# Kernel tuning notes

Measured on AMD Instinct MI355X. Metric: run time of the kernel, lower is better.

## Reference

```python
import jax, jax.numpy as jnp
import numpy as np

N, F, H, D = 50000, 128, 8, 16   # nodes, node features, heads, per-head dim (F == H*D -> Identity residual)
E, G = 800000, 512               # edges, graphs
HD = H * D


def _xavier(key, shape):
    fan = sum(shape[-2:]) if len(shape) >= 2 else shape[0] + 1
    lim = (6.0 / (shape[-2] + shape[-1])) ** 0.5 if len(shape) >= 2 else (6.0 / fan) ** 0.5
    return jax.random.uniform(key, shape, jnp.float32, -lim, lim)


def setup_inputs() -> dict:
    key = jax.random.key(0)
    ks = jax.random.split(key, 10)
    x = jax.random.normal(ks[0], (N, F), jnp.float32)
    edge_index = jax.random.randint(ks[1], (2, E), 0, N, dtype=jnp.int64)
    batch = jnp.sort(jax.random.randint(ks[2], (N,), 0, G, dtype=jnp.int64))
    W_src = _xavier(ks[3], (HD, F))
    W_dst = _xavier(ks[4], (HD, F))
    double_attn = _xavier(ks[5], (1, H, D))  # xavier over last two dims
    bias = jnp.zeros((HD,), jnp.float32)
    prelu_alpha = jnp.float32(0.25)          # nn.PReLU() default single weight
    w_weighting = _xavier(ks[6], (1, HD))
    b_weighting = jnp.zeros((1,), jnp.float32)
    w_score = _xavier(ks[7], (HD, HD))
    b_score = jnp.zeros((HD,), jnp.float32)
    return {
        "x": x, "edge_index": edge_index, "batch": batch,
        "W_src": W_src, "W_dst": W_dst, "double_attn": double_attn,
        "bias": bias, "prelu_alpha": prelu_alpha,
        "w_weighting": w_weighting, "b_weighting": b_weighting,
        "w_score": w_score, "b_score": b_score,
    }


def reference(x, edge_index, batch, W_src, W_dst, double_attn, bias, prelu_alpha,
              w_weighting, b_weighting, w_score, b_score):
    src, dst = edge_index[0], edge_index[1]
    # dropout is identity in eval mode
    src_p = (x @ W_src.T).reshape(N, H, D)    # [N,H,D]
    dst_p = (x @ W_dst.T).reshape(N, H, D)
    # edge-wise attention logits: gather + LeakyReLU(0.2) + dot with attention vector
    e = src_p[src] + dst_p[dst]               # [E,H,D]
    e = jnp.where(e > 0, e, 0.2 * e)
    logits = jnp.einsum('ehd,ohd->eh', e, double_attn)  # [E,H] (double_attn has leading 1)
    # segment softmax over destination nodes (global max shift, as in original)
    exp = jnp.exp(logits - logits.max())
    denom = jax.ops.segment_sum(exp, dst, num_segments=N)  # [N,H]
    alpha = exp / (denom[dst] + 1e-16)        # [E,H]
    # weighted aggregation of source projections
    msg = src_p[src] * alpha[:, :, None]      # [E,H,D]
    out = jax.ops.segment_sum(msg, dst, num_segments=N)    # [N,H,D]
    out = out + x.reshape(N, H, D)            # residual (Identity since F == H*D)
    out = out.reshape(N, HD) + bias           # concat heads + bias
    out = jnp.where(out > 0, out, prelu_alpha * out)       # PReLU activation
    # ReadoutPhase: gated sum pooling + max pooling per graph, concatenated
    weighted = jax.nn.sigmoid(out @ w_weighting.T + b_weighting)  # [N,1]
    score = out @ w_score.T + b_score                              # [N,HD]
    g_sum = jax.ops.segment_sum(weighted * score, batch, num_segments=G)  # [G,HD]
    g_max = jax.ops.segment_max(out, batch, num_segments=G)              # [G,HD]
    readout = jnp.concatenate([g_sum, g_max], axis=1)                     # [G,2*HD]
    return out, readout
```

## Files before the change

### kernel.cpp

```cpp
#include <hip/hip_runtime.h>

#define NODES 50000
#define FEAT 128
#define EDGES 800000
#define GRAPHS 512
#define NB 196
#define CHUNK 4096
#define ABLK 196
#define BCAP 8192
#define PROJ_BLOCKS 782

typedef unsigned int u32;
typedef unsigned short u16;
typedef __attribute__((ext_vector_type(8))) short short8;
typedef __attribute__((ext_vector_type(4))) float v4f;
typedef __attribute__((ext_vector_type(4))) u32 u32x4;
typedef __attribute__((ext_vector_type(2))) float f2;

static __device__ __forceinline__ float bflo(u32 u){ return __uint_as_float(u << 16); }
static __device__ __forceinline__ float bfhi(u32 u){ return __uint_as_float(u & 0xffff0000u); }
static __device__ __forceinline__ u16 f2bf(float f){
  u32 u = __float_as_uint(f);
  u32 r = u + 0x7fffu + ((u >> 16) & 1u);
  return (u16)(r >> 16);
}
static __device__ __forceinline__ u32 packbf(float a, float b){
  return (u32)f2bf(a) | ((u32)f2bf(b) << 16);
}
static __device__ __forceinline__ f2 unpk(u32 u){ f2 r; r.x = bflo(u); r.y = bfhi(u); return r; }
static __device__ __forceinline__ f2 vmax2(f2 a, f2 b){ f2 r; r.x = fmaxf(a.x,b.x); r.y = fmaxf(a.y,b.y); return r; }

#define LROW 68
__global__ __launch_bounds__(256) void proj_hist_kernel(
    const float* __restrict__ x, const float* __restrict__ Wsrc,
    const float* __restrict__ Wdst, u16* __restrict__ srcp, u16* __restrict__ dstp,
    const int* __restrict__ ei, int* __restrict__ bcount)
{
  __shared__ u32 x_lds[64 * LROW];
  __shared__ int cnt[NB];
  const int t = threadIdx.x;

  if (blockIdx.x >= PROJ_BLOCKS){
    const int b = blockIdx.x - PROJ_BLOCKS;
    for (int k = t; k < NB; k += 256) cnt[k] = 0;
    __syncthreads();
    const int e0 = b * CHUNK;
    const int e1 = (e0 + CHUNK < EDGES) ? e0 + CHUNK : EDGES;
    for (int e = e0 + t; e < e1; e += 256)
      atomicAdd(&cnt[ei[EDGES + e] >> 8], 1);
    __syncthreads();
    for (int k = t; k < NB; k += 256) bcount[b * NB + k] = cnt[k];
    return;
  }

  const int node0 = blockIdx.x * 64;
  const int rows_valid = NODES - node0 < 64 ? NODES - node0 : 64;
  const float4* xp = (const float4*)(x + (size_t)node0 * 128);
  for (int idx = t; idx < rows_valid * 32; idx += 256){
    const float4 v = xp[idx];
    const int row = idx >> 5, cq = idx & 31;
    x_lds[row * LROW + cq * 2]     = packbf(v.x, v.y);
    x_lds[row * LROW + cq * 2 + 1] = packbf(v.z, v.w);
  }

  const int wave = t >> 6, lane = t & 63;
  const int r16 = lane & 15;
  const int quad = lane >> 4;
  const int ko = quad * 4;
  const int n0 = wave * 32;

  short8 bs[2][4], bd[2][4];
  #pragma unroll
  for (int nt = 0; nt < 2; ++nt){
    const int col = n0 + nt * 16 + r16;
    #pragma unroll
    for (int k = 0; k < 4; ++k){
      const float4* wp = (const float4*)(Wsrc + col * 128 + quad * 8 + k * 32);
      float4 w0 = wp[0], w1 = wp[1];
      u32x4 pk; pk.x = packbf(w0.x,w0.y); pk.y = packbf(w0.z,w0.w);
      pk.z = packbf(w1.x,w1.y); pk.w = packbf(w1.z,w1.w);
      bs[nt][k] = __builtin_bit_cast(short8, pk);
      const float4* vp = (const float4*)(Wdst + col * 128 + quad * 8 + k * 32);
      float4 v0 = vp[0], v1 = vp[1];
      u32x4 qk; qk.x = packbf(v0.x,v0.y); qk.y = packbf(v0.z,v0.w);
      qk.z = packbf(v1.x,v1.y); qk.w = packbf(v1.z,v1.w);
      bd[nt][k] = __builtin_bit_cast(short8, qk);
    }
  }
  __syncthreads();

  #pragma unroll
  for (int mt = 0; mt < 4; ++mt){
    const int node_base = node0 + mt * 16;
    if (node_base >= NODES) break;
    short8 afr[4];
    #pragma unroll
    for (int k = 0; k < 4; ++k)
      afr[k] = *(const short8*)&x_lds[(mt * 16 + r16) * LROW + ko + k * 16];
    v4f s0 = {0.f,0.f,0.f,0.f}, s1 = s0, d0 = s0, d1 = s0;
    #pragma unroll
    for (int k = 0; k < 4; ++k){
      s0 = __builtin_amdgcn_mfma_f32_16x16x32_bf16(afr[k], bs[0][k], s0, 0, 0, 0);
      s1 = __builtin_amdgcn_mfma_f32_16x16x32_bf16(afr[k], bs[1][k], s1, 0, 0, 0);
      d0 = __builtin_amdgcn_mfma_f32_16x16x32_bf16(afr[k], bd[0][k], d0, 0, 0, 0);
      d1 = __builtin_amdgcn_mfma_f32_16x16x32_bf16(afr[k], bd[1][k], d1, 0, 0, 0);
    }
    const int node = node_base + quad * 4;
    u16* so0 = srcp + ((size_t)(wave*2)   * NODES + node) * 16 + r16;
    u16* so1 = srcp + ((size_t)(wave*2+1) * NODES + node) * 16 + r16;
    u16* dd0 = dstp + ((size_t)(wave*2)   * NODES + node) * 16 + r16;
    u16* dd1 = dstp + ((size_t)(wave*2+1) * NODES + node) * 16 + r16;
    #pragma unroll
    for (int r = 0; r < 4; ++r){
      so0[r * 16] = f2bf(s0[r]);
      so1[r * 16] = f2bf(s1[r]);
      dd0[r * 16] = f2bf(d0[r]);
      dd1[r * 16] = f2bf(d1[r]);
    }
  }
}

__global__ __launch_bounds__(256) void bucket_scatter_kernel(
    const int* __restrict__ ei, const int* __restrict__ bcount,
    int* __restrict__ bstart_g, u32* __restrict__ ebuf, float* __restrict__ wsum)
{
  __shared__ int tot[256];
  __shared__ int bstart_s[NB + 1];
  __shared__ int obase_s[NB];
  __shared__ int cur[NB];
  const int b = blockIdx.x, t = threadIdx.x;
  const int nid = b * 256 + t;
  if (nid < NODES) wsum[nid] = 0.f;
  int total = 0, obase = 0;
  if (t < NB){
    int run = 0;
    for (int q = 0; q < ABLK; ++q){
      if (q == b) obase = run;
      run += bcount[q * NB + t];
    }
    total = run;
  }
  tot[t] = total;
  __syncthreads();
  const int v = total;
  for (int off = 1; off < 256; off <<= 1){
    const int add = (t >= off) ? tot[t - off] : 0;
    __syncthreads();
    tot[t] += add;
    __syncthreads();
  }
  if (t < NB){
    bstart_s[t] = tot[t] - v;
    obase_s[t] = obase;
    cur[t] = 0;
  }
  if (t == NB - 1) bstart_s[NB] = tot[t];
  __syncthreads();
  if (b == 0 && t <= NB) bstart_g[t] = bstart_s[t];

  const int e0 = b * CHUNK;
  const int e1 = (e0 + CHUNK < EDGES) ? e0 + CHUNK : EDGES;
  for (int e = e0 + t; e < e1; e += 256){
    const int d = ei[EDGES + e];
    const int s = ei[e];
    const int k = d >> 8;
    const int r = atomicAdd(&cur[k], 1);
    ebuf[bstart_s[k] + obase_s[k] + r] = (u32)s | ((u32)(d & 255) << 16);
  }
}

__global__ __launch_bounds__(256) void bucket_csr_kernel(
    const u32* __restrict__ ebuf, const int* __restrict__ bstart,
    int* __restrict__ row_start, u16* __restrict__ srclist)
{
  __shared__ int cnt[256], excl[256], cur[256];
  __shared__ u32 loc[BCAP];
  const int k = blockIdx.x, t = threadIdx.x;
  const int base = bstart[k];
  int ne = bstart[k + 1] - base;
  if (ne > BCAP) ne = BCAP;
  cnt[t] = 0;
  __syncthreads();
  for (int j = t; j < ne; j += 256)
    atomicAdd(&cnt[(ebuf[base + j] >> 16) & 255], 1);
  __syncthreads();
  const int v = cnt[t];
  for (int off = 1; off < 256; off <<= 1){
    const int add = (t >= off) ? cnt[t - off] : 0;
    __syncthreads();
    cnt[t] += add;
    __syncthreads();
  }
  excl[t] = cnt[t] - v;
  cur[t] = cnt[t] - v;
  __syncthreads();
  const int node = k * 256 + t;
  if (node <= NODES) row_start[node] = base + excl[t];
  for (int j = t; j < ne; j += 256){
    const u32 e = ebuf[base + j];
    const int p = atomicAdd(&cur[(e >> 16) & 255], 1);
    loc[p] = e & 0xFFFFu;
  }
  __syncthreads();
  for (int j = t; j < ne; j += 256)
    srclist[base + j] = (u16)loc[j];
}

__global__ __launch_bounds__(256) void aggregate_kernel(
    const u16* __restrict__ srcp, const u16* __restrict__ dstp,
    const int* __restrict__ row_start, const u16* __restrict__ srclist,
    const float* __restrict__ x, const float* __restrict__ attn,
    const float* __restrict__ bias, const float* __restrict__ palpha,
    const float* __restrict__ ww, float* __restrict__ outp,
    float* __restrict__ wsum)
{
  const int h   = blockIdx.x & 7;
  const int grp = blockIdx.x >> 3;
  const int wv = threadIdx.x >> 6;
  const int lane = threadIdx.x & 63;
  const int half = lane >> 5;
  const int l32 = lane & 31;
  const int es = l32 >> 1;
  const int dh = lane & 1;
  const int i = grp * 8 + wv * 2 + half;
  const size_t hN = (size_t)h * NODES;
  const uint4* sp = (const uint4*)srcp;

  f2 d2[4], a2[4];
  {
    const uint4 dv = ((const uint4*)dstp)[(hN + i) * 2 + dh];
    d2[0]=unpk(dv.x); d2[1]=unpk(dv.y); d2[2]=unpk(dv.z); d2[3]=unpk(dv.w);
    const float4* ap = (const float4*)(attn + h * 16 + dh * 8);
    const float4 a0 = ap[0], a1 = ap[1];
    a2[0].x=a0.x; a2[0].y=a0.y; a2[1].x=a0.z; a2[1].y=a0.w;
    a2[2].x=a1.x; a2[2].y=a1.y; a2[3].x=a1.z; a2[3].y=a1.w;
  }
  const int lo = row_start[i], hi = row_start[i + 1];
  const int deg = hi - lo;
  int myidx = 0;
  if (l32 < deg) myidx = (int)srclist[lo + l32];
  const int nb = (deg + 15) >> 4;
  int nbw = nb; { const int o = __shfl_xor(nb, 32); if (o > nbw) nbw = o; }

  f2 acc[4];
  #pragma unroll
  for (int q = 0; q < 4; ++q){ acc[q].x = 0.f; acc[q].y = 0.f; }
  float denom = 0.f;

  auto COMP = [&](bool valid, const uint4& A){
    f2 sv[4];
    sv[0]=unpk(A.x); sv[1]=unpk(A.y); sv[2]=unpk(A.z); sv[3]=unpk(A.w);
    f2 p; p.x = 0.f; p.y = 0.f;
    #pragma unroll
    for (int q = 0; q < 4; ++q){
      f2 e = sv[q] + d2[q];
      e = vmax2(e, e * 0.2f);
      p += e * a2[q];
    }
    const float p8 = p.x + p.y;
    const float lg = p8 + __shfl_xor(p8, 1);
    const float w = valid ? __expf(lg) : 0.f;
    denom += w;
    f2 w2; w2.x = w; w2.y = w;
    #pragma unroll
    for (int q = 0; q < 4; ++q) acc[q] += sv[q] * w2;
  };

  int s0, s1; bool v0, v1;
  { const int j = es;      v0 = j < deg; const int t0 = __shfl(myidx, half*32 + j); s0 = v0 ? t0 : 0; }
  { const int j = 16 + es; v1 = j < deg; const int t1 = __shfl(myidx, half*32 + j); s1 = v1 ? t1 : 0; }

  uint4 A0, A1;
  if (nbw > 0) A0 = sp[(hN + s0) * 2 + dh];
  if (nbw > 1) A1 = sp[(hN + s1) * 2 + dh];
  if (nbw > 0) COMP(v0, A0);
  if (nbw > 1) COMP(v1, A1);
  if (nbw > 2){
    for (int c = 2; c < nbw; ++c){
      const int j = c * 16 + es;
      const bool v = j < deg;
      const int s = v ? (int)srclist[lo + j] : 0;
      const uint4 A = sp[(hN + s) * 2 + dh];
      COMP(v, A);
    }
  }

  #pragma unroll
  for (int m = 2; m <= 16; m <<= 1) denom += __shfl_xor(denom, m);

  float af[8];
  af[0]=acc[0].x; af[1]=acc[0].y; af[2]=acc[1].x; af[3]=acc[1].y;
  af[4]=acc[2].x; af[5]=acc[2].y; af[6]=acc[3].x; af[7]=acc[3].y;
  float b4[4];
  #pragma unroll
  for (int k = 0; k < 4; ++k){
    const float give = (lane & 2) ? af[k] : af[4 + k];
    const float got = __shfl_xor(give, 2);
    b4[k] = ((lane & 2) ? af[4 + k] : af[k]) + got;
  }
  float c2[2];
  #pragma unroll
  for (int k = 0; k < 2; ++k){
    const float give = (lane & 4) ? b4[k] : b4[2 + k];
    const float got = __shfl_xor(give, 4);
    c2[k] = ((lane & 4) ? b4[2 + k] : b4[k]) + got;
  }
  float d1;
  {
    const float give = (lane & 8) ? c2[0] : c2[1];
    const float got = __shfl_xor(give, 8);
    d1 = ((lane & 8) ? c2[1] : c2[0]) + got;
  }
  d1 += __shfl_xor(d1, 16);

  const float inv = 1.f / (denom + 1e-16f);
  const int dim = dh * 8 + ((lane & 2) ? 4 : 0) + ((lane & 4) ? 2 : 0) + ((lane & 8) ? 1 : 0);
  const int col = h * 16 + dim;
  const float xr = x[(size_t)i * 128 + col];
  const float bv = bias[col];
  const float al = palpha[0];
  float tv = fmaf(d1, inv, xr) + bv;
  const float o = (tv > 0.f) ? tv : al * tv;
  if ((lane & 16) == 0) outp[(size_t)i * 128 + col] = o;

  float z = (lane & 16) ? 0.f : o * ww[col];
  z += __shfl_xor(z, 1); z += __shfl_xor(z, 2); z += __shfl_xor(z, 4);
  z += __shfl_xor(z, 8); z += __shfl_xor(z, 16);
  if (l32 == 0) atomicAdd(&wsum[i], z);
}

__global__ __launch_bounds__(256) void readout_kernel(
    const float* __restrict__ outp, const float* __restrict__ wsumv,
    const int* __restrict__ batchv, const float* __restrict__ bw,
    const float* __restrict__ wscore, const float* __restrict__ bscore,
    float* __restrict__ ro)
{
  __shared__ int range_s[2];
  __shared__ float wsum_s[128];
  __shared__ float max_s[128];
  __shared__ float wtot_s[2];
  __shared__ float part_s[256];
  const int g = blockIdx.x, t = threadIdx.x;
  const int col = t & 127, grp = t >> 7;
  const float bw0 = bw[0];
  if (t < 2){
    const int target = g + t;
    int lo = 0, hi = NODES;
    while (lo < hi){ const int m = (lo + hi) >> 1; if (batchv[m] < target) lo = m + 1; else hi = m; }
    range_s[t] = lo;
  }
  __syncthreads();
  const int lo = range_s[0], hi = range_s[1];
  float acc = 0.f, vmax = -INFINITY, wacc = 0.f;
  for (int n = lo + grp; n < hi; n += 2){
    const float w = 1.f / (1.f + __expf(-(wsumv[n] + bw0)));
    const float v = outp[n * 128 + col];
    acc = fmaf(w, v, acc);
    vmax = fmaxf(vmax, v);
    if (col == 0) wacc += w;
  }
  part_s[t] = acc;
  if (col == 0) wtot_s[grp] = wacc;
  __syncthreads();
  if (grp == 0) wsum_s[col] = acc + part_s[col + 128];
  __syncthreads();
  part_s[t] = vmax;
  __syncthreads();
  if (grp == 0) max_s[col] = fmaxf(vmax, part_s[col + 128]);
  const float wtot = wtot_s[0] + wtot_s[1];
  __syncthreads();
  float dot = 0.f;
  const float* wr = wscore + col * 128 + grp * 64;
  const float* xs = wsum_s + grp * 64;
  #pragma unroll
  for (int k = 0; k < 64; ++k) dot = fmaf(wr[k], xs[k], dot);
  part_s[t] = dot;
  __syncthreads();
  if (grp == 0){
    const float s = dot + part_s[col + 128] + wtot * bscore[col];
    ro[g * 256 + col] = s;
    ro[g * 256 + 128 + col] = max_s[col];
  }
}

extern "C" void kernel_launch(void* const* d_in, const int* in_sizes, int n_in,
                              void* d_out, int out_size, void* d_ws, size_t ws_size,
                              hipStream_t stream)
{
  const float* x      = (const float*)d_in[0];
  const int*   ei     = (const int*)d_in[1];
  const int*   batchv = (const int*)d_in[2];
  const float* Wsrc   = (const float*)d_in[3];
  const float* Wdst   = (const float*)d_in[4];
  const float* attn   = (const float*)d_in[5];
  const float* bias   = (const float*)d_in[6];
  const float* palpha = (const float*)d_in[7];
  const float* ww     = (const float*)d_in[8];
  const float* bw     = (const float*)d_in[9];
  const float* wsc    = (const float*)d_in[10];
  const float* bsc    = (const float*)d_in[11];

  char* ws = (char*)d_ws;
  u16*  srcp      = (u16*) (ws + 0);
  u16*  dstp      = (u16*) (ws + 12800000);
  u16*  srclist   = (u16*) (ws + 25600000);
  int*  row_start = (int*) (ws + 28800000);
  int*  bcount    = (int*) (ws + 29000192);
  int*  bstart    = (int*) (ws + 29153856);
  float* wsum     = (float*)(ws + 29154688);

  float* outp = (float*)d_out;
  float* ro = outp + NODES * FEAT;
  u32* ebuf = (u32*)d_out;

  proj_hist_kernel<<<PROJ_BLOCKS + ABLK, 256, 0, stream>>>(
      x, Wsrc, Wdst, srcp, dstp, ei, bcount);
  bucket_scatter_kernel<<<ABLK, 256, 0, stream>>>(ei, bcount, bstart, ebuf, wsum);
  bucket_csr_kernel<<<NB, 256, 0, stream>>>(ebuf, bstart, row_start, srclist);
  aggregate_kernel<<<(NODES / 8) * 8, 256, 0, stream>>>(srcp, dstp, row_start, srclist,
                                                        x, attn, bias, palpha, ww,
                                                        outp, wsum);
  readout_kernel<<<GRAPHS, 256, 0, stream>>>(outp, wsum, batchv, bw, wsc, bsc, ro);
}
```

Baseline: 255.6 us.

## Remap aggregate kernel to 8 lanes per node with full-row edge loads

```diff
diff --git a/kernel.cpp b/kernel.cpp
--- a/kernel.cpp
+++ b/kernel.cpp
@@ -206,7 +206,7 @@
     srclist[base + j] = (u16)loc[j];
 }
 
-__global__ __launch_bounds__(256) void aggregate_kernel(
+__global__ __launch_bounds__(256, 4) void aggregate_kernel(
     const u16* __restrict__ srcp, const u16* __restrict__ dstp,
     const int* __restrict__ row_start, const u16* __restrict__ srclist,
     const float* __restrict__ x, const float* __restrict__ attn,
@@ -218,115 +218,134 @@
   const int grp = blockIdx.x >> 3;
   const int wv = threadIdx.x >> 6;
   const int lane = threadIdx.x & 63;
-  const int half = lane >> 5;
-  const int l32 = lane & 31;
-  const int es = l32 >> 1;
-  const int dh = lane & 1;
-  const int i = grp * 8 + wv * 2 + half;
+  const int nd = lane >> 3;
+  const int es = lane & 7;
+  const int i = grp * 32 + wv * 8 + nd;
+  const bool vn = i < NODES;
+  const int ic = vn ? i : NODES - 1;
   const size_t hN = (size_t)h * NODES;
   const uint4* sp = (const uint4*)srcp;
 
-  f2 d2[4], a2[4];
+  f2 d2[8], a2[8];
   {
-    const uint4 dv = ((const uint4*)dstp)[(hN + i) * 2 + dh];
-    d2[0]=unpk(dv.x); d2[1]=unpk(dv.y); d2[2]=unpk(dv.z); d2[3]=unpk(dv.w);
-    const float4* ap = (const float4*)(attn + h * 16 + dh * 8);
-    const float4 a0 = ap[0], a1 = ap[1];
-    a2[0].x=a0.x; a2[0].y=a0.y; a2[1].x=a0.z; a2[1].y=a0.w;
-    a2[2].x=a1.x; a2[2].y=a1.y; a2[3].x=a1.z; a2[3].y=a1.w;
-  }
-  const int lo = row_start[i], hi = row_start[i + 1];
+    const uint4 dA = ((const uint4*)dstp)[(hN + ic) * 2];
+    const uint4 dB = ((const uint4*)dstp)[(hN + ic) * 2 + 1];
+    d2[0]=unpk(dA.x); d2[1]=unpk(dA.y); d2[2]=unpk(dA.z); d2[3]=unpk(dA.w);
+    d2[4]=unpk(dB.x); d2[5]=unpk(dB.y); d2[6]=unpk(dB.z); d2[7]=unpk(dB.w);
+    const float4* ap = (const float4*)(attn + h * 16);
+    const float4 a0 = ap[0], a1 = ap[1], a2v = ap[2], a3v = ap[3];
+    a2[0].x=a0.x;  a2[0].y=a0.y;  a2[1].x=a0.z;  a2[1].y=a0.w;
+    a2[2].x=a1.x;  a2[2].y=a1.y;  a2[3].x=a1.z;  a2[3].y=a1.w;
+    a2[4].x=a2v.x; a2[4].y=a2v.y; a2[5].x=a2v.z; a2[5].y=a2v.w;
+    a2[6].x=a3v.x; a2[6].y=a3v.y; a2[7].x=a3v.z; a2[7].y=a3v.w;
+  }
+  const int lo = vn ? row_start[i] : 0;
+  const int hi = vn ? row_start[i + 1] : 0;
   const int deg = hi - lo;
-  int myidx = 0;
-  if (l32 < deg) myidx = (int)srclist[lo + l32];
-  const int nb = (deg + 15) >> 4;
-  int nbw = nb; { const int o = __shfl_xor(nb, 32); if (o > nbw) nbw = o; }
-
-  f2 acc[4];
-  #pragma unroll
-  for (int q = 0; q < 4; ++q){ acc[q].x = 0.f; acc[q].y = 0.f; }
+  const int nb = (deg + 7) >> 3;
+  int nbw = nb;
+  { int o = __shfl_xor(nbw, 8);  if (o > nbw) nbw = o; }
+  { int o = __shfl_xor(nbw, 16); if (o > nbw) nbw = o; }
+  { int o = __shfl_xor(nbw, 32); if (o > nbw) nbw = o; }
+
+  f2 acc[8];
+  #pragma unroll
+  for (int q = 0; q < 8; ++q){ acc[q].x = 0.f; acc[q].y = 0.f; }
   float denom = 0.f;
 
-  auto COMP = [&](bool valid, const uint4& A){
-    f2 sv[4];
+  auto FETCH = [&](int c, uint4& A, uint4& B, bool& v){
+    const int j = c * 8 + es;
+    v = j < deg;
+    const int s = v ? (int)srclist[lo + j] : 0;
+    const uint4* rp = sp + (hN + s) * 2;
+    A = rp[0]; B = rp[1];
+  };
+  auto COMP = [&](bool v, const uint4& A, const uint4& B){
+    f2 sv[8];
     sv[0]=unpk(A.x); sv[1]=unpk(A.y); sv[2]=unpk(A.z); sv[3]=unpk(A.w);
+    sv[4]=unpk(B.x); sv[5]=unpk(B.y); sv[6]=unpk(B.z); sv[7]=unpk(B.w);
     f2 p; p.x = 0.f; p.y = 0.f;
     #pragma unroll
-    for (int q = 0; q < 4; ++q){
+    for (int q = 0; q < 8; ++q){
       f2 e = sv[q] + d2[q];
       e = vmax2(e, e * 0.2f);
       p += e * a2[q];
     }
-    const float p8 = p.x + p.y;
-    const float lg = p8 + __shfl_xor(p8, 1);
-    const float w = valid ? __expf(lg) : 0.f;
+    const float w = v ? __expf(p.x + p.y) : 0.f;
     denom += w;
     f2 w2; w2.x = w; w2.y = w;
     #pragma unroll
-    for (int q = 0; q < 4; ++q) acc[q] += sv[q] * w2;
+    for (int q = 0; q < 8; ++q) acc[q] += sv[q] * w2;
   };
 
-  int s0, s1; bool v0, v1;
-  { const int j = es;      v0 = j < deg; const int t0 = __shfl(myidx, half*32 + j); s0 = v0 ? t0 : 0; }
-  { const int j = 16 + es; v1 = j < deg; const int t1 = __shfl(myidx, half*32 + j); s1 = v1 ? t1 : 0; }
-
-  uint4 A0, A1;
-  if (nbw > 0) A0 = sp[(hN + s0) * 2 + dh];
-  if (nbw > 1) A1 = sp[(hN + s1) * 2 + dh];
-  if (nbw > 0) COMP(v0, A0);
-  if (nbw > 1) COMP(v1, A1);
-  if (nbw > 2){
-    for (int c = 2; c < nbw; ++c){
-      const int j = c * 16 + es;
-      const bool v = j < deg;
-      const int s = v ? (int)srclist[lo + j] : 0;
-      const uint4 A = sp[(hN + s) * 2 + dh];
-      COMP(v, A);
-    }
-  }
-
-  #pragma unroll
-  for (int m = 2; m <= 16; m <<= 1) denom += __shfl_xor(denom, m);
-
-  float af[8];
-  af[0]=acc[0].x; af[1]=acc[0].y; af[2]=acc[1].x; af[3]=acc[1].y;
-  af[4]=acc[2].x; af[5]=acc[2].y; af[6]=acc[3].x; af[7]=acc[3].y;
-  float b4[4];
-  #pragma unroll
-  for (int k = 0; k < 4; ++k){
-    const float give = (lane & 2) ? af[k] : af[4 + k];
-    const float got = __shfl_xor(give, 2);
-    b4[k] = ((lane & 2) ? af[4 + k] : af[k]) + got;
-  }
-  float c2[2];
-  #pragma unroll
-  for (int k = 0; k < 2; ++k){
-    const float give = (lane & 4) ? b4[k] : b4[2 + k];
-    const float got = __shfl_xor(give, 4);
-    c2[k] = ((lane & 4) ? b4[2 + k] : b4[k]) + got;
-  }
-  float d1;
+  uint4 A0, B0, A1, B1; bool v0 = false, v1 = false;
+  if (nbw > 0) FETCH(0, A0, B0, v0);
+  if (nbw > 1) FETCH(1, A1, B1, v1);
+  if (nbw > 0){ COMP(v0, A0, B0); if (nbw > 2) FETCH(2, A0, B0, v0); }
+  if (nbw > 1){ COMP(v1, A1, B1); if (nbw > 3) FETCH(3, A1, B1, v1); }
+  if (nbw > 2) COMP(v0, A0, B0);
+  if (nbw > 3) COMP(v1, A1, B1);
+  if (nbw > 4){
+    for (int c = 4; c < nbw; ++c){
+      uint4 TA, TB; bool tv;
+      FETCH(c, TA, TB, tv);
+      COMP(tv, TA, TB);
+    }
+  }
+
+  denom += __shfl_xor(denom, 1);
+  denom += __shfl_xor(denom, 2);
+  denom += __shfl_xor(denom, 4);
+  const float inv = 1.f / (denom + 1e-16f);
+
+  float v8[8];
+  #pragma unroll
+  for (int q = 0; q < 4; ++q){
+    const float gx = (es & 4) ? acc[q].x : acc[4 + q].x;
+    const float gy = (es & 4) ? acc[q].y : acc[4 + q].y;
+    const float rx = __shfl_xor(gx, 4);
+    const float ry = __shfl_xor(gy, 4);
+    v8[2*q]   = ((es & 4) ? acc[4 + q].x : acc[q].x) + rx;
+    v8[2*q+1] = ((es & 4) ? acc[4 + q].y : acc[q].y) + ry;
+  }
+  float v4a[4];
+  #pragma unroll
+  for (int q = 0; q < 2; ++q){
+    const float gx = (es & 2) ? v8[2*q]   : v8[4 + 2*q];
+    const float gy = (es & 2) ? v8[2*q+1] : v8[4 + 2*q+1];
+    const float rx = __shfl_xor(gx, 2);
+    const float ry = __shfl_xor(gy, 2);
+    v4a[2*q]   = ((es & 2) ? v8[4 + 2*q]   : v8[2*q]) + rx;
+    v4a[2*q+1] = ((es & 2) ? v8[4 + 2*q+1] : v8[2*q+1]) + ry;
+  }
+  float r0, r1;
   {
-    const float give = (lane & 8) ? c2[0] : c2[1];
-    const float got = __shfl_xor(give, 8);
-    d1 = ((lane & 8) ? c2[1] : c2[0]) + got;
-  }
-  d1 += __shfl_xor(d1, 16);
-
-  const float inv = 1.f / (denom + 1e-16f);
-  const int dim = dh * 8 + ((lane & 2) ? 4 : 0) + ((lane & 4) ? 2 : 0) + ((lane & 8) ? 1 : 0);
-  const int col = h * 16 + dim;
-  const float xr = x[(size_t)i * 128 + col];
-  const float bv = bias[col];
+    const float g0 = (es & 1) ? v4a[0] : v4a[2];
+    const float g1 = (es & 1) ? v4a[1] : v4a[3];
+    const float q0 = __shfl_xor(g0, 1);
+    const float q1 = __shfl_xor(g1, 1);
+    r0 = ((es & 1) ? v4a[2] : v4a[0]) + q0;
+    r1 = ((es & 1) ? v4a[3] : v4a[1]) + q1;
+  }
+
+  const int col = h * 16 + es * 2;
+  const f2 xr = *(const f2*)(x + (size_t)ic * 128 + col);
+  const f2 bv = *(const f2*)(bias + col);
   const float al = palpha[0];
-  float tv = fmaf(d1, inv, xr) + bv;
-  const float o = (tv > 0.f) ? tv : al * tv;
-  if ((lane & 16) == 0) outp[(size_t)i * 128 + col] = o;
-
-  float z = (lane & 16) ? 0.f : o * ww[col];
-  z += __shfl_xor(z, 1); z += __shfl_xor(z, 2); z += __shfl_xor(z, 4);
-  z += __shfl_xor(z, 8); z += __shfl_xor(z, 16);
-  if (l32 == 0) atomicAdd(&wsum[i], z);
+  const float t0 = fmaf(r0, inv, xr.x) + bv.x;
+  const float t1 = fmaf(r1, inv, xr.y) + bv.y;
+  const float o0 = (t0 > 0.f) ? t0 : al * t0;
+  const float o1 = (t1 > 0.f) ? t1 : al * t1;
+  if (vn){
+    f2 ov; ov.x = o0; ov.y = o1;
+    *(f2*)(outp + (size_t)i * 128 + col) = ov;
+  }
+  const f2 gv = *(const f2*)(ww + col);
+  float z = o0 * gv.x + o1 * gv.y;
+  z += __shfl_xor(z, 1);
+  z += __shfl_xor(z, 2);
+  z += __shfl_xor(z, 4);
+  if (vn && es == 0) atomicAdd(&wsum[i], z);
 }
 
 __global__ __launch_bounds__(256) void readout_kernel(
@@ -417,8 +436,9 @@
       x, Wsrc, Wdst, srcp, dstp, ei, bcount);
   bucket_scatter_kernel<<<ABLK, 256, 0, stream>>>(ei, bcount, bstart, ebuf, wsum);
   bucket_csr_kernel<<<NB, 256, 0, stream>>>(ebuf, bstart, row_start, srclist);
-  aggregate_kernel<<<(NODES / 8) * 8, 256, 0, stream>>>(srcp, dstp, row_start, srclist,
-                                                        x, attn, bias, palpha, ww,
-                                                        outp, wsum);
+  const int ngrp = (NODES + 31) / 32;
+  aggregate_kernel<<<ngrp * 8, 256, 0, stream>>>(srcp, dstp, row_start, srclist,
+                                                 x, attn, bias, palpha, ww,
+                                                 outp, wsum);
   readout_kernel<<<GRAPHS, 256, 0, stream>>>(outp, wsum, batchv, bw, wsc, bsc, ro);
 }
```

New measurement: 223.9 us. 1.14x faster.
